# Optimization experiments

Hardware: AMD Instinct MI355X
Metric: run time of the kernel (lower is better)

The kernel has to match this reference:

```python
import jax, jax.numpy as jnp
import numpy as np

B, N1, N2, DEG = 64, 512, 512, 16
NF, NH, NL = 128, 128, 3
RATIO = 0.5
K1 = int(np.ceil(RATIO * N1))
K2 = int(np.ceil(RATIO * N2))
NCLS = 2
NCAT = NH * NL  # 384


def _gl(key, shape, fan_in):
    return jax.random.normal(key, shape, jnp.float32) / np.sqrt(fan_in)


def setup_inputs() -> dict:
    key = jax.random.key(0)
    ks = jax.random.split(key, 24)
    x = jax.random.normal(ks[0], (B * (N1 + N2), NF), jnp.float32)
    # edges within each component of each graph (c1-local / c2-local and global indexing)
    s1 = jax.random.randint(ks[1], (B, N1 * DEG), 0, N1)
    d1 = jax.random.randint(ks[2], (B, N1 * DEG), 0, N1)
    s2 = jax.random.randint(ks[3], (B, N2 * DEG), 0, N2)
    d2 = jax.random.randint(ks[4], (B, N2 * DEG), 0, N2)
    off1 = (jnp.arange(B) * N1)[:, None]
    off2 = (jnp.arange(B) * N2)[:, None]
    offg = (jnp.arange(B) * (N1 + N2))[:, None]
    src_c1 = (s1 + off1).reshape(-1).astype(jnp.int32)
    dst_c1 = (d1 + off1).reshape(-1).astype(jnp.int32)
    src_c2 = (s2 + off2).reshape(-1).astype(jnp.int32)
    dst_c2 = (d2 + off2).reshape(-1).astype(jnp.int32)
    src_all = jnp.concatenate([(s1 + offg).reshape(-1), (s2 + N1 + offg).reshape(-1)]).astype(jnp.int32)
    dst_all = jnp.concatenate([(d1 + offg).reshape(-1), (d2 + N1 + offg).reshape(-1)]).astype(jnp.int32)
    return {
        'x': x,
        'src_all': src_all, 'dst_all': dst_all,
        'src_c1': src_c1, 'dst_c1': dst_c1,
        'src_c2': src_c2, 'dst_c2': dst_c2,
        'W1': _gl(ks[5], (NF, NH), NF), 'b1': jnp.zeros((NH,), jnp.float32),
        'W2': _gl(ks[6], (NH, NH), NH), 'b2': jnp.zeros((NH,), jnp.float32),
        'W3': _gl(ks[7], (NH, NH), NH), 'b3': jnp.zeros((NH,), jnp.float32),
        'Wg_att': _gl(ks[8], (NCAT, NCAT), NCAT),
        'Wal': _gl(ks[9], (2 * NCAT, 2 * NCAT), 2 * NCAT), 'bal': jnp.zeros((2 * NCAT,), jnp.float32),
        'Wf': _gl(ks[10], (NCAT, NH), NCAT), 'bf': jnp.zeros((NH,), jnp.float32),
        'Wg_fin': _gl(ks[11], (NH, NH), NH),
        'Wl1': _gl(ks[12], (2 * NH, NH), 2 * NH), 'bl1': jnp.zeros((NH,), jnp.float32),
        'Wl2': _gl(ks[13], (NH, NH // 2), NH), 'bl2': jnp.zeros((NH // 2,), jnp.float32),
        'Wl3': _gl(ks[14], (NH // 2, NCLS), NH // 2), 'bl3': jnp.zeros((NCLS,), jnp.float32),
    }


def gcn_conv(x, src, dst, emask, W, b, n):
    # PyG GCNConv: symmetric norm with self-loops; masked edges contribute zero.
    xw = x @ W
    w = emask.astype(x.dtype)
    src_s = jnp.where(emask, src, 0)
    dst_s = jnp.where(emask, dst, 0)
    deg = jax.ops.segment_sum(w, dst_s, num_segments=n) + 1.0  # +1 self-loop
    dis = jax.lax.rsqrt(deg)
    norm = dis[src_s] * dis[dst_s] * w
    out = jax.ops.segment_sum(xw[src_s] * norm[:, None], dst_s, num_segments=n)
    out = out + xw * (dis * dis)[:, None]  # self-loop message
    return out + b


def att_pool(x, batch, counts, Wg, nseg):
    # global_pool with cfg 'ATT': gap -> tanh(W) -> broadcast -> sigmoid gate -> sum pool
    mean = jax.ops.segment_sum(x, batch, num_segments=nseg) / counts[:, None]
    c = jnp.tanh(mean @ Wg)
    alpha = jax.nn.sigmoid(jnp.sum(x * c[batch], axis=1, keepdims=True))
    return jax.ops.segment_sum(x * alpha, batch, num_segments=nseg)


def cag_pool(xc, src, dst, pv, n_per, k):
    # CAGPool_layer: score = <x, pool_vec>/||pool_vec||, per-graph topk, gate by sigmoid(score)
    batch = jnp.repeat(jnp.arange(B), n_per)
    x_ = pv[batch]
    score = jnp.sum(xc * x_, axis=1) / jnp.linalg.norm(x_, axis=1)
    order = jnp.argsort(-score.reshape(B, n_per), axis=1)[:, :k]
    perm = (order + (jnp.arange(B) * n_per)[:, None]).reshape(-1)  # [B*k]
    pooled = xc[perm] * jax.nn.sigmoid(score[perm])[:, None]
    # filter_adj: remap kept nodes, mask out edges touching dropped nodes
    node_map = jnp.full((B * n_per,), -1, dtype=jnp.int32).at[perm].set(jnp.arange(B * k, dtype=jnp.int32))
    r, c = node_map[src], node_map[dst]
    emask = (r >= 0) & (c >= 0)
    return pooled, r, c, emask


def reference(x, src_all, dst_all, src_c1, dst_c1, src_c2, dst_c2,
              W1, b1, W2, b2, W3, b3, Wg_att, Wal, bal, Wf, bf, Wg_fin,
              Wl1, bl1, Wl2, bl2, Wl3, bl3):
    N = B * (N1 + N2)
    ones_all = jnp.ones(src_all.shape[0], dtype=bool)
    h = jax.nn.relu(gcn_conv(x, src_all, dst_all, ones_all, W1, b1, N))
    xs = [h]
    for W, b in ((W2, b2), (W3, b3)):
        h = jax.nn.relu(gcn_conv(h, src_all, dst_all, ones_all, W, b, N))
        xs.append(h)
    xcat = jnp.concatenate(xs, axis=1)  # [N, NCAT]
    # split combined node set into c1 / c2 components (static layout)
    offg = (jnp.arange(B) * (N1 + N2))[:, None]
    idx1 = (offg + jnp.arange(N1)[None, :]).reshape(-1)
    idx2 = (offg + N1 + jnp.arange(N2)[None, :]).reshape(-1)
    x_c1, x_c2 = xcat[idx1], xcat[idx2]
    batch_c1 = jnp.repeat(jnp.arange(B), N1)
    batch_c2 = jnp.repeat(jnp.arange(B), N2)
    x12 = jnp.concatenate([x_c1, x_c2], axis=0)
    batch_ = jnp.concatenate([batch_c1, batch_c2 + B])
    counts = jnp.concatenate([jnp.full((B,), N1, jnp.float32), jnp.full((B,), N2, jnp.float32)])
    gp = att_pool(x12, batch_, counts, Wg_att, 2 * B)
    pv = jnp.concatenate([gp[:B], gp[B:]], axis=1) @ Wal + bal  # att_lin
    pv1, pv2 = pv[:, :NCAT], pv[:, NCAT:]
    p1, r1, c1e, m1 = cag_pool(x_c1, src_c1, dst_c1, pv1, N1, K1)
    p2, r2, c2e, m2 = cag_pool(x_c2, src_c2, dst_c2, pv2, N2, K2)
    h1 = jax.nn.relu(gcn_conv(p1, r1, c1e, m1, Wf, bf, B * K1))
    h2 = jax.nn.relu(gcn_conv(p2, r2, c2e, m2, Wf, bf, B * K2))
    g1 = att_pool(h1, jnp.repeat(jnp.arange(B), K1), jnp.full((B,), K1, jnp.float32), Wg_fin, B)
    g2 = att_pool(h2, jnp.repeat(jnp.arange(B), K2), jnp.full((B,), K2, jnp.float32), Wg_fin, B)
    pred = jnp.concatenate([g1, g2], axis=1)
    pred = jax.nn.relu(pred @ Wl1 + bl1)
    pred = jax.nn.relu(pred @ Wl2 + bl2)
    return pred @ Wl3 + bl3  # [B, NCLS]
```

## Files before the change

kernel.cpp:

```cpp
#include <hip/hip_runtime.h>
#include <math.h>

constexpr int BB   = 64;
constexpr int NPB  = 1024;
constexpr int NN   = BB * NPB;
constexpr int EALL = 1048576;
constexpr int EC   = 524288;
constexpr int EPG  = 8192;
constexpr int KTOP = 256;
constexpr int NP   = BB * KTOP;
constexpr int NP2  = 2 * NP;

__device__ __forceinline__ int wswz(int q) { return q ^ ((q >> 3) & 1); }

__global__ __launch_bounds__(256) void k_build_csr(const int* __restrict__ src_all,
                                                   const int* __restrict__ dst_all,
                                                   int* __restrict__ rowstart,
                                                   int* __restrict__ csrc,
                                                   float* __restrict__ dis) {
    __shared__ int cnt[512];
    __shared__ int rs[512];
    __shared__ int wsum[4];
    __shared__ int stage[EPG];
    const int g = blockIdx.x;
    const int b = g >> 1, c = g & 1;
    const int ebase  = c * EC + b * EPG;
    const int region = g * EPG;
    const int nbase  = g * 512;
    const int t = threadIdx.x;
    const int lane = t & 63, w = t >> 6;

    cnt[t] = 0; cnt[t + 256] = 0;
    __syncthreads();
    for (int i = 0; i < 32; i++) {
        int d = dst_all[ebase + t + 256 * i] & 511;
        atomicAdd(&cnt[d], 1);
    }
    __syncthreads();
    int v0 = cnt[2 * t], v1 = cnt[2 * t + 1];
    int p = v0 + v1;
    int incl = p;
    for (int off = 1; off < 64; off <<= 1) {
        int u = __shfl_up(incl, off);
        if (lane >= off) incl += u;
    }
    if (lane == 63) wsum[w] = incl;
    __syncthreads();
    int base = 0;
    for (int i = 0; i < w; i++) base += wsum[i];
    int excl = base + incl - p;
    rs[2 * t] = excl;
    rs[2 * t + 1] = excl + v0;
    rowstart[nbase + 2 * t]     = region + excl;
    rowstart[nbase + 2 * t + 1] = region + excl + v0;
    dis[nbase + 2 * t]     = 1.0f / sqrtf((float)v0 + 1.0f);
    dis[nbase + 2 * t + 1] = 1.0f / sqrtf((float)v1 + 1.0f);
    if (g == 127 && t == 0) rowstart[NN] = EALL;
    __syncthreads();
    for (int i = 0; i < 32; i++) {
        int e = ebase + t + 256 * i;
        int d = dst_all[e] & 511;
        int pp = atomicAdd(&rs[d], 1);
        stage[pp] = src_all[e];
    }
    __syncthreads();
    for (int i = 0; i < 32; i++)
        csrc[region + t + 256 * i] = stage[t + 256 * i];
}

__global__ __launch_bounds__(256) void k_build_csr_pooled(const int* __restrict__ s1,
                                                          const int* __restrict__ d1,
                                                          const int* __restrict__ s2,
                                                          const int* __restrict__ d2,
                                                          const int* __restrict__ nmap,
                                                          int* __restrict__ rowstart,
                                                          int* __restrict__ cntp,
                                                          int* __restrict__ csre,
                                                          float* __restrict__ disp) {
    __shared__ int cnt[256];
    __shared__ int rs[256];
    __shared__ int wsum[4];
    __shared__ int stage[EPG];
    const int g = blockIdx.x;
    const int c = g >> 6, b = g & 63;
    const int* ss = c ? s2 : s1;
    const int* dd = c ? d2 : d1;
    const int* nm = nmap + c * 32768;
    const int ebase  = b * EPG;
    const int region = g * EPG;
    const int nbase  = g * 256;
    const int t = threadIdx.x;
    const int lane = t & 63, w = t >> 6;

    cnt[t] = 0;
    __syncthreads();
    for (int i = 0; i < 32; i++) {
        int e = ebase + t + 256 * i;
        int r = nm[ss[e]], cc = nm[dd[e]];
        if (r >= 0 && cc >= 0) atomicAdd(&cnt[cc & 255], 1);
    }
    __syncthreads();
    int v = cnt[t];
    int incl = v;
    for (int off = 1; off < 64; off <<= 1) {
        int u = __shfl_up(incl, off);
        if (lane >= off) incl += u;
    }
    if (lane == 63) wsum[w] = incl;
    __syncthreads();
    int base = 0;
    for (int i = 0; i < w; i++) base += wsum[i];
    int excl = base + incl - v;
    rs[t] = excl;
    rowstart[nbase + t] = region + excl;
    cntp[nbase + t] = v;
    disp[nbase + t] = 1.0f / sqrtf((float)v + 1.0f);
    __syncthreads();
    for (int i = 0; i < 32; i++) {
        int e = ebase + t + 256 * i;
        int r = nm[ss[e]], cc = nm[dd[e]];
        if (r >= 0 && cc >= 0) {
            int pp = atomicAdd(&rs[cc & 255], 1);
            stage[pp] = r;
        }
    }
    __syncthreads();
    for (int i = 0; i < 32; i++)
        csre[region + t + 256 * i] = stage[t + 256 * i];
}

template <int KDIM>
__global__ __launch_bounds__(256) void k_gemm_tile(const float* __restrict__ A, int lda,
                                                   const float* __restrict__ W,
                                                   const float* __restrict__ rowscale,
                                                   float* __restrict__ C, int M) {
    __shared__ float As[32][136];
    __shared__ float Ws[32 * 128];
    const int tid  = threadIdx.x;
    const int c0 = (tid & 15) * 8;
    const int r0 = (tid >> 4) * 8;
    const int row0 = blockIdx.x * 128;
    const int arow = tid >> 1;
    const int aq   = tid & 1;

    float acc[8][8];
#pragma unroll
    for (int i = 0; i < 8; i++)
#pragma unroll
        for (int j = 0; j < 8; j++) acc[i][j] = 0.f;

    for (int k0 = 0; k0 < KDIM; k0 += 32) {
        __syncthreads();
        const float* Ap = A + (size_t)(row0 + arow) * lda + k0;
#pragma unroll
        for (int qq = 0; qq < 4; qq++) {
            int kk = (aq + 2 * qq) * 4;
            float4 av = *(const float4*)(Ap + kk);
            As[kk + 0][arow] = av.x;
            As[kk + 1][arow] = av.y;
            As[kk + 2][arow] = av.z;
            As[kk + 3][arow] = av.w;
        }
#pragma unroll
        for (int q = 0; q < 4; q++) {
            int f = tid + 256 * q;
            int kk = f >> 5, qd = f & 31;
            float4 wv = *(const float4*)(W + (size_t)k0 * 128 + f * 4);
            *(float4*)&Ws[kk * 128 + wswz(qd) * 4] = wv;
        }
        __syncthreads();
#pragma unroll 2
        for (int kk = 0; kk < 32; kk++) {
            int q0 = c0 >> 2;
            float4 a0 = *(const float4*)&As[kk][r0];
            float4 a1 = *(const float4*)&As[kk][r0 + 4];
            float4 b0 = *(const float4*)&Ws[kk * 128 + wswz(q0) * 4];
            float4 b1 = *(const float4*)&Ws[kk * 128 + wswz(q0 + 1) * 4];
            float a[8] = {a0.x, a0.y, a0.z, a0.w, a1.x, a1.y, a1.z, a1.w};
            float b[8] = {b0.x, b0.y, b0.z, b0.w, b1.x, b1.y, b1.z, b1.w};
#pragma unroll
            for (int i = 0; i < 8; i++)
#pragma unroll
                for (int j = 0; j < 8; j++)
                    acc[i][j] = fmaf(a[i], b[j], acc[i][j]);
        }
    }
#pragma unroll
    for (int i = 0; i < 8; i++) {
        int row = row0 + r0 + i;
        if (row < M) {
            float sc = rowscale[row];
            float4 o0 = {acc[i][0]*sc, acc[i][1]*sc, acc[i][2]*sc, acc[i][3]*sc};
            float4 o1 = {acc[i][4]*sc, acc[i][5]*sc, acc[i][6]*sc, acc[i][7]*sc};
            *(float4*)(C + (size_t)row * 128 + c0) = o0;
            *(float4*)(C + (size_t)row * 128 + c0 + 4) = o1;
        }
    }
}

__global__ __launch_bounds__(512) void k_gemm_gather(const float* __restrict__ XC,
                                                     const int* __restrict__ sel,
                                                     const float* __restrict__ SC,
                                                     const float* __restrict__ rowscale,
                                                     const float* __restrict__ W,
                                                     float* __restrict__ C) {
    __shared__ float As[32][136];
    __shared__ float Ws[32 * 128];
    const int tid  = threadIdx.x;
    const int c0 = (tid & 15) * 8;
    const int r0 = (tid >> 4) * 4;
    const int row0 = blockIdx.x * 128;
    const int arow = tid >> 2;
    const int aq   = tid & 3;

    int n = row0 + arow;
    int comm = n >= NP;
    int nl = n - (comm ? NP : 0);
    int b = nl >> 8;
    int old = sel[n];
    const float* srow = XC + (size_t)(b * NPB + comm * 512 + old) * 384;
    float scv = SC[comm * 32768 + b * 512 + old];
    float sg = 1.f / (1.f + expf(-scv));

    float acc[4][8];
#pragma unroll
    for (int i = 0; i < 4; i++)
#pragma unroll
        for (int j = 0; j < 8; j++) acc[i][j] = 0.f;

    for (int k0 = 0; k0 < 384; k0 += 32) {
        __syncthreads();
#pragma unroll
        for (int qq = 0; qq < 2; qq++) {
            int kk = (aq + 4 * qq) * 4;
            float4 av = *(const float4*)(srow + k0 + kk);
            As[kk + 0][arow] = av.x * sg;
            As[kk + 1][arow] = av.y * sg;
            As[kk + 2][arow] = av.z * sg;
            As[kk + 3][arow] = av.w * sg;
        }
#pragma unroll
        for (int q = 0; q < 2; q++) {
            int f = tid + 512 * q;
            int kk = f >> 5, qd = f & 31;
            float4 wv = *(const float4*)(W + (size_t)k0 * 128 + f * 4);
            *(float4*)&Ws[kk * 128 + wswz(qd) * 4] = wv;
        }
        __syncthreads();
#pragma unroll 2
        for (int kk = 0; kk < 32; kk++) {
            int q0 = c0 >> 2;
            float4 a0 = *(const float4*)&As[kk][r0];
            float4 b0 = *(const float4*)&Ws[kk * 128 + wswz(q0) * 4];
            float4 b1 = *(const float4*)&Ws[kk * 128 + wswz(q0 + 1) * 4];
            float a[4] = {a0.x, a0.y, a0.z, a0.w};
            float b8[8] = {b0.x, b0.y, b0.z, b0.w, b1.x, b1.y, b1.z, b1.w};
#pragma unroll
            for (int i = 0; i < 4; i++)
#pragma unroll
                for (int j = 0; j < 8; j++)
                    acc[i][j] = fmaf(a[i], b8[j], acc[i][j]);
        }
    }
#pragma unroll
    for (int i = 0; i < 4; i++) {
        int row = row0 + r0 + i;
        float sc = rowscale[row];
        float4 o0 = {acc[i][0]*sc, acc[i][1]*sc, acc[i][2]*sc, acc[i][3]*sc};
        float4 o1 = {acc[i][4]*sc, acc[i][5]*sc, acc[i][6]*sc, acc[i][7]*sc};
        *(float4*)(C + (size_t)row * 128 + c0) = o0;
        *(float4*)(C + (size_t)row * 128 + c0 + 4) = o1;
    }
}

__global__ void k_aggregate4(const float* __restrict__ xwsc, const float* __restrict__ dis,
                             const int* __restrict__ rowstart, const int* __restrict__ csrc,
                             const float* __restrict__ bias, float* __restrict__ XC, int colbase) {
    int xcd  = blockIdx.x & 7;
    int slot = blockIdx.x >> 3;
    int g    = ((slot >> 6) << 3) | xcd;
    int node = g * 512 + (slot & 63) * 8 + (threadIdx.x >> 5);
    int l    = threadIdx.x & 31;
    const float4* xw4 = (const float4*)xwsc;
    float4 acc = xw4[(size_t)node * 32 + l];
    int e0 = rowstart[node], e1 = rowstart[node + 1];
    for (int e = e0; e < e1; e++) {
        int s = csrc[e];
        float4 u = xw4[(size_t)s * 32 + l];
        acc.x += u.x; acc.y += u.y; acc.z += u.z; acc.w += u.w;
    }
    float di = dis[node];
    float4 b4 = ((const float4*)bias)[l];
    acc.x = fmaxf(acc.x * di + b4.x, 0.f);
    acc.y = fmaxf(acc.y * di + b4.y, 0.f);
    acc.z = fmaxf(acc.z * di + b4.z, 0.f);
    acc.w = fmaxf(acc.w * di + b4.w, 0.f);
    *(float4*)(XC + (size_t)node * 384 + colbase + l * 4) = acc;
}

__global__ void k_aggregate_pooled(const float* __restrict__ xwsc, const float* __restrict__ disp,
                                   const int* __restrict__ rowstart, const int* __restrict__ cntp,
                                   const int* __restrict__ csre,
                                   const float* __restrict__ bias, float* __restrict__ H) {
    int xcd  = blockIdx.x & 7;
    int slot = blockIdx.x >> 3;
    int g    = ((slot >> 5) << 3) | xcd;
    int node = g * 256 + (slot & 31) * 8 + (threadIdx.x >> 5);
    int l    = threadIdx.x & 31;
    const float4* xw4 = (const float4*)xwsc;
    float4 acc = xw4[(size_t)node * 32 + l];
    int e0 = rowstart[node], n = cntp[node];
    for (int i = 0; i < n; i++) {
        int r = csre[e0 + i];
        float4 u = xw4[(size_t)r * 32 + l];
        acc.x += u.x; acc.y += u.y; acc.z += u.z; acc.w += u.w;
    }
    float di = disp[node];
    float4 b4 = ((const float4*)bias)[l];
    acc.x = fmaxf(acc.x * di + b4.x, 0.f);
    acc.y = fmaxf(acc.y * di + b4.y, 0.f);
    acc.z = fmaxf(acc.z * di + b4.z, 0.f);
    acc.w = fmaxf(acc.w * di + b4.w, 0.f);
    *(float4*)(H + (size_t)node * 128 + l * 4) = acc;
}

__global__ void k_mean_part(const float* __restrict__ XC, float* __restrict__ mpart) {
    int blk = blockIdx.x;
    int gc = blk >> 2, p = blk & 3;
    int seg = ((gc & 1) << 6) | (gc >> 1);
    int c = threadIdx.x;
    int base = gc * 512 + p * 128;
    float s = 0.f;
    for (int i = 0; i < 128; i++) s += XC[(size_t)(base + i) * 384 + c];
    mpart[(size_t)(seg * 4 + p) * 384 + c] = s;
}

__global__ void k_c12(const float* __restrict__ mpart, const float* __restrict__ Wg,
                      float* __restrict__ c12) {
    __shared__ float ms[384];
    int seg = blockIdx.x; int c = threadIdx.x;
    ms[c] = (mpart[(size_t)(seg * 4 + 0) * 384 + c] + mpart[(size_t)(seg * 4 + 1) * 384 + c] +
             mpart[(size_t)(seg * 4 + 2) * 384 + c] + mpart[(size_t)(seg * 4 + 3) * 384 + c]) *
            (1.0f / 512.0f);
    __syncthreads();
    float s = 0.f;
    for (int k = 0; k < 384; k++) s = fmaf(ms[k], Wg[(size_t)k * 384 + c], s);
    c12[seg * 384 + c] = tanhf(s);
}

__global__ __launch_bounds__(256) void k_attpool1(const float* __restrict__ XC,
                                                  const float* __restrict__ C12,
                                                  float* __restrict__ GP) {
    __shared__ float gps[4][384];
    int blk = blockIdx.x;
    int gc = blk >> 2, q = blk & 3;
    int seg = ((gc & 1) << 6) | (gc >> 1);
    int w = threadIdx.x >> 6, l = threadIdx.x & 63;
    const float* c12r = C12 + seg * 384;
    float4 cr0 = *(const float4*)(c12r + 4 * l);
    float4 cr1 = (l < 32) ? *(const float4*)(c12r + 256 + 4 * l) : float4{0.f,0.f,0.f,0.f};
    float4 a0 = {0.f,0.f,0.f,0.f}, a1 = {0.f,0.f,0.f,0.f};
    int base = gc * 512 + q * 128 + w * 32;
    for (int it = 0; it < 32; it++) {
        const float* xr = XC + (size_t)(base + it) * 384;
        float4 v0 = *(const float4*)(xr + 4 * l);
        float4 v1 = (l < 32) ? *(const float4*)(xr + 256 + 4 * l) : float4{0.f,0.f,0.f,0.f};
        float s = v0.x*cr0.x + v0.y*cr0.y + v0.z*cr0.z + v0.w*cr0.w
                + v1.x*cr1.x + v1.y*cr1.y + v1.z*cr1.z + v1.w*cr1.w;
        for (int off = 32; off; off >>= 1) s += __shfl_xor(s, off);
        float al = 1.f / (1.f + expf(-s));
        a0.x += v0.x*al; a0.y += v0.y*al; a0.z += v0.z*al; a0.w += v0.w*al;
        a1.x += v1.x*al; a1.y += v1.y*al; a1.z += v1.z*al; a1.w += v1.w*al;
    }
    *(float4*)&gps[w][4 * l] = a0;
    if (l < 32) *(float4*)&gps[w][256 + 4 * l] = a1;
    __syncthreads();
    for (int c = threadIdx.x; c < 384; c += 256) {
        float s = gps[0][c] + gps[1][c] + gps[2][c] + gps[3][c];
        atomicAdd(&GP[seg * 384 + c], s);
    }
}

__global__ void k_pv(const float* __restrict__ gp, const float* __restrict__ Wal,
                     const float* __restrict__ bal, float* __restrict__ pv) {
    int row = blockIdx.x;
    int c   = threadIdx.x;
    float s = bal[c];
    for (int k = 0; k < 768; k++) {
        float v = (k < 384) ? gp[row * 384 + k] : gp[(64 + row) * 384 + (k - 384)];
        s = fmaf(v, Wal[(size_t)k * 768 + c], s);
    }
    pv[row * 768 + c] = s;
}

__global__ void k_pnorm(const float* __restrict__ pv, float* __restrict__ pnorm) {
    int id = blockIdx.x;
    int lane = threadIdx.x;
    int h = id >> 6, b = id & 63;
    const float* p = pv + b * 768 + h * 384;
    float s = 0.f;
    for (int k = lane; k < 384; k += 64) s += p[k] * p[k];
    for (int off = 32; off; off >>= 1) s += __shfl_down(s, off);
    if (lane == 0) pnorm[id] = sqrtf(s);
}

__global__ void k_score(const float* __restrict__ XC, const float* __restrict__ pv,
                        const float* __restrict__ pnorm, float* __restrict__ sc) {
    int nl2 = blockIdx.x * 4 + (threadIdx.x >> 6);
    int lane = threadIdx.x & 63;
    int comm = nl2 >> 15;
    int nl = nl2 & 32767;
    int b = nl >> 9; int i = nl & 511;
    const float* xr = XC + (size_t)(b * NPB + comm * 512 + i) * 384;
    const float* pr = pv + b * 768 + comm * 384;
    float4 x0 = *(const float4*)(xr + 4 * lane);
    float4 p0 = *(const float4*)(pr + 4 * lane);
    float s = x0.x*p0.x + x0.y*p0.y + x0.z*p0.z + x0.w*p0.w;
    if (lane < 32) {
        float4 x1 = *(const float4*)(xr + 256 + 4 * lane);
        float4 p1 = *(const float4*)(pr + 256 + 4 * lane);
        s += x1.x*p1.x + x1.y*p1.y + x1.z*p1.z + x1.w*p1.w;
    }
    for (int off = 32; off; off >>= 1) s += __shfl_down(s, off);
    if (lane == 0) sc[comm * 32768 + nl] = s / pnorm[comm * 64 + b];
}

__global__ void k_topk(const float* __restrict__ sc, int* __restrict__ sel, int* __restrict__ nmap) {
    __shared__ float sv[512];
    __shared__ int   si[512];
    int blk = blockIdx.x;
    int t = threadIdx.x;
    sv[t] = sc[blk * 512 + t];             si[t] = t;
    sv[t + 256] = sc[blk * 512 + t + 256]; si[t + 256] = t + 256;
    __syncthreads();
    for (int k2 = 2; k2 <= 512; k2 <<= 1) {
        for (int j = k2 >> 1; j > 0; j >>= 1) {
            for (int i = t; i < 512; i += 256) {
                int l = i ^ j;
                if (l > i) {
                    bool desc = ((i & k2) == 0);
                    float a = sv[i], bb2 = sv[l];
                    bool sw = desc ? (a < bb2) : (a > bb2);
                    if (sw) {
                        sv[i] = bb2; sv[l] = a;
                        int tmp = si[i]; si[i] = si[l]; si[l] = tmp;
                    }
                }
            }
            __syncthreads();
        }
    }
    sel[blk * 256 + t] = si[t];
    nmap[blk * 512 + si[t]] = blk * 256 + t;
    nmap[blk * 512 + si[t + 256]] = -1;
}

__global__ void k_meanf(const float* __restrict__ H, float* __restrict__ mean) {
    int b = blockIdx.x; int c = threadIdx.x;
    float s = 0.f;
    for (int i = 0; i < 256; i++) s += H[(size_t)(b * 256 + i) * 128 + c];
    mean[b * 128 + c] = s * (1.0f / 256.0f);
}

__global__ void k_cfin(const float* __restrict__ mean, const float* __restrict__ Wg,
                       float* __restrict__ cf) {
    __shared__ float ms[128];
    int b = blockIdx.x; int c = threadIdx.x;
    ms[c] = mean[b * 128 + c];
    __syncthreads();
    float s = 0.f;
    for (int k = 0; k < 128; k++) s = fmaf(ms[k], Wg[k * 128 + c], s);
    cf[b * 128 + c] = tanhf(s);
}

__global__ void k_alphaf(const float* __restrict__ H, const float* __restrict__ cf,
                         float* __restrict__ al) {
    int node = blockIdx.x * 4 + (threadIdx.x >> 6);
    int lane = threadIdx.x & 63;
    int b = node >> 8;
    float s = 0.f;
    if (lane < 32) {
        float4 h = *(const float4*)(H + (size_t)node * 128 + 4 * lane);
        float4 c = *(const float4*)(cf + b * 128 + 4 * lane);
        s = h.x*c.x + h.y*c.y + h.z*c.z + h.w*c.w;
    }
    for (int off = 32; off; off >>= 1) s += __shfl_down(s, off);
    if (lane == 0) al[node] = 1.f / (1.f + expf(-s));
}

__global__ void k_gfin(const float* __restrict__ H, const float* __restrict__ al,
                       float* __restrict__ g) {
    int seg = blockIdx.x; int c = threadIdx.x;
    int b = seg & 63, comm = seg >> 6;
    float s = 0.f;
    for (int i = 0; i < 256; i++) { int n = seg * 256 + i; s += H[(size_t)n * 128 + c] * al[n]; }
    g[b * 256 + comm * 128 + c] = s;
}

__global__ void k_mlp(const float* __restrict__ G,
                      const float* __restrict__ Wl1, const float* __restrict__ bl1,
                      const float* __restrict__ Wl2, const float* __restrict__ bl2,
                      const float* __restrict__ Wl3, const float* __restrict__ bl3,
                      float* __restrict__ out) {
    __shared__ float t1[128], t2[64];
    int b = blockIdx.x; int t = threadIdx.x;
    float s = bl1[t];
    for (int k = 0; k < 256; k++) s = fmaf(G[b * 256 + k], Wl1[k * 128 + t], s);
    t1[t] = fmaxf(s, 0.f);
    __syncthreads();
    if (t < 64) {
        float s2 = bl2[t];
        for (int k = 0; k < 128; k++) s2 = fmaf(t1[k], Wl2[k * 64 + t], s2);
        t2[t] = fmaxf(s2, 0.f);
    }
    __syncthreads();
    if (t < 2) {
        float s3 = bl3[t];
        for (int k = 0; k < 64; k++) s3 = fmaf(t2[k], Wl3[k * 2 + t], s3);
        out[b * 2 + t] = s3;
    }
}

extern "C" void kernel_launch(void* const* d_in, const int* in_sizes, int n_in,
                              void* d_out, int out_size, void* d_ws, size_t ws_size,
                              hipStream_t stream) {
    const float* x       = (const float*)d_in[0];
    const int*   src_all = (const int*)d_in[1];
    const int*   dst_all = (const int*)d_in[2];
    const int*   src_c1  = (const int*)d_in[3];
    const int*   dst_c1  = (const int*)d_in[4];
    const int*   src_c2  = (const int*)d_in[5];
    const int*   dst_c2  = (const int*)d_in[6];
    const float* W1 = (const float*)d_in[7];   const float* b1 = (const float*)d_in[8];
    const float* W2 = (const float*)d_in[9];   const float* b2 = (const float*)d_in[10];
    const float* W3 = (const float*)d_in[11];  const float* b3 = (const float*)d_in[12];
    const float* Wg_att = (const float*)d_in[13];
    const float* Wal = (const float*)d_in[14]; const float* bal = (const float*)d_in[15];
    const float* Wf  = (const float*)d_in[16]; const float* bf  = (const float*)d_in[17];
    const float* Wg_fin = (const float*)d_in[18];
    const float* Wl1 = (const float*)d_in[19]; const float* bl1 = (const float*)d_in[20];
    const float* Wl2 = (const float*)d_in[21]; const float* bl2 = (const float*)d_in[22];
    const float* Wl3 = (const float*)d_in[23]; const float* bl3 = (const float*)d_in[24];
    float* out = (float*)d_out;

    float* f = (float*)d_ws;
    size_t o = 0;
    float* XC   = f + o; o += (size_t)NN * 384;
    float* SCR  = f + o; o += (size_t)NN * 128;
    float* H    = f + o; o += (size_t)NP2 * 128;
    int* ROWSTART = (int*)(f + o); o += 65552;
    int* CSRC     = (int*)(f + o); o += EALL;
    int* CNTP     = (int*)(f + o); o += NP2;
    float* DIS    = f + o; o += NN;
    float* MPART  = f + o; o += 512 * 384;
    float* C12    = f + o; o += 128 * 384;
    float* GP     = f + o; o += 128 * 384;
    float* PV     = f + o; o += 64 * 768;
    float* PNORM  = f + o; o += 128;
    float* SC     = f + o; o += 65536;
    int* SEL      = (int*)(f + o); o += NP2;
    int* NMAP     = (int*)(f + o); o += 65536;
    float* DISP   = f + o; o += NP2;
    float* MEANF  = f + o; o += 128 * 128;
    float* CFIN   = f + o; o += 128 * 128;
    float* ALF    = f + o; o += NP2;
    float* G12    = f + o; o += 64 * 256;
    size_t needed_bytes = o * sizeof(float);
    if (ws_size < needed_bytes) return;

    float* XWP = SCR;

    k_build_csr<<<128, 256, 0, stream>>>(src_all, dst_all, ROWSTART, CSRC, DIS);

    k_gemm_tile<128><<<NN / 128, 256, 0, stream>>>(x, 128, W1, DIS, SCR, NN);
    k_aggregate4<<<NN / 8, 256, 0, stream>>>(SCR, DIS, ROWSTART, CSRC, b1, XC, 0);
    k_gemm_tile<128><<<NN / 128, 256, 0, stream>>>(XC + 0, 384, W2, DIS, SCR, NN);
    k_aggregate4<<<NN / 8, 256, 0, stream>>>(SCR, DIS, ROWSTART, CSRC, b2, XC, 128);
    k_gemm_tile<128><<<NN / 128, 256, 0, stream>>>(XC + 128, 384, W3, DIS, SCR, NN);
    k_aggregate4<<<NN / 8, 256, 0, stream>>>(SCR, DIS, ROWSTART, CSRC, b3, XC, 256);

    k_mean_part<<<512, 384, 0, stream>>>(XC, MPART);
    k_c12<<<128, 384, 0, stream>>>(MPART, Wg_att, C12);
    hipMemsetAsync(GP, 0, 128 * 384 * sizeof(float), stream);
    k_attpool1<<<512, 256, 0, stream>>>(XC, C12, GP);
    k_pv<<<64, 768, 0, stream>>>(GP, Wal, bal, PV);
    k_pnorm<<<128, 64, 0, stream>>>(PV, PNORM);

    k_score<<<65536 / 4, 256, 0, stream>>>(XC, PV, PNORM, SC);
    k_topk<<<128, 256, 0, stream>>>(SC, SEL, NMAP);

    k_build_csr_pooled<<<128, 256, 0, stream>>>(src_c1, dst_c1, src_c2, dst_c2,
                                                NMAP, ROWSTART, CNTP, CSRC, DISP);

    k_gemm_gather<<<NP2 / 128, 512, 0, stream>>>(XC, SEL, SC, DISP, Wf, XWP);
    k_aggregate_pooled<<<NP2 / 8, 256, 0, stream>>>(XWP, DISP, ROWSTART, CNTP, CSRC, bf, H);

    k_meanf<<<128, 128, 0, stream>>>(H, MEANF);
    k_cfin<<<128, 128, 0, stream>>>(MEANF, Wg_fin, CFIN);
    k_alphaf<<<NP2 / 4, 256, 0, stream>>>(H, CFIN, ALF);
    k_gfin<<<128, 128, 0, stream>>>(H, ALF, G12);

    k_mlp<<<64, 128, 0, stream>>>(G12, Wl1, bl1, Wl2, bl2, Wl3, bl3, out);
}
```

Measured before the change: 631.1 us.

## Double-buffer shared-memory tiles with register prefetch in GEMM kernels

Both tiled GEMM kernels now use two shared-memory buffers. The next K-tile is loaded from global memory into registers while the current tile is computed, then written to the other buffer, so there is one barrier per iteration instead of two. The W swizzle becomes a full XOR (q ^ (q>>3)) and the A padding drops from 136 to 132 to change the LDS bank mapping. This doubles LDS use and adds prefetch registers, which may lower occupancy.

```diff
diff --git a/kernel.cpp b/kernel.cpp
--- a/kernel.cpp
+++ b/kernel.cpp
@@ -11,7 +11,7 @@
 constexpr int NP   = BB * KTOP;
 constexpr int NP2  = 2 * NP;
 
-__device__ __forceinline__ int wswz(int q) { return q ^ ((q >> 3) & 1); }
+__device__ __forceinline__ int pq(int q) { return q ^ (q >> 3); }
 
 __global__ __launch_bounds__(256) void k_build_csr(const int* __restrict__ src_all,
                                                    const int* __restrict__ dst_all,
@@ -134,14 +134,17 @@
                                                    const float* __restrict__ W,
                                                    const float* __restrict__ rowscale,
                                                    float* __restrict__ C, int M) {
-    __shared__ float As[32][136];
-    __shared__ float Ws[32 * 128];
+    __shared__ float As[2][32][132];
+    __shared__ float Ws[2][32 * 128];
     const int tid  = threadIdx.x;
     const int c0 = (tid & 15) * 8;
     const int r0 = (tid >> 4) * 8;
     const int row0 = blockIdx.x * 128;
     const int arow = tid >> 1;
     const int aq   = tid & 1;
+    const float* Ap = A + (size_t)(row0 + arow) * lda;
+    const int pq0 = pq(c0 >> 2) * 4;
+    const int pq1 = pq((c0 >> 2) + 1) * 4;
 
     float acc[8][8];
 #pragma unroll
@@ -149,33 +152,50 @@
 #pragma unroll
         for (int j = 0; j < 8; j++) acc[i][j] = 0.f;
 
-    for (int k0 = 0; k0 < KDIM; k0 += 32) {
-        __syncthreads();
-        const float* Ap = A + (size_t)(row0 + arow) * lda + k0;
-#pragma unroll
-        for (int qq = 0; qq < 4; qq++) {
-            int kk = (aq + 2 * qq) * 4;
-            float4 av = *(const float4*)(Ap + kk);
-            As[kk + 0][arow] = av.x;
-            As[kk + 1][arow] = av.y;
-            As[kk + 2][arow] = av.z;
-            As[kk + 3][arow] = av.w;
-        }
-#pragma unroll
-        for (int q = 0; q < 4; q++) {
-            int f = tid + 256 * q;
-            int kk = f >> 5, qd = f & 31;
-            float4 wv = *(const float4*)(W + (size_t)k0 * 128 + f * 4);
-            *(float4*)&Ws[kk * 128 + wswz(qd) * 4] = wv;
-        }
-        __syncthreads();
+    float4 areg[4], wreg[4];
+#pragma unroll
+    for (int qq = 0; qq < 4; qq++)
+        areg[qq] = *(const float4*)(Ap + (aq + 2 * qq) * 4);
+#pragma unroll
+    for (int q = 0; q < 4; q++) {
+        int f = tid + 256 * q;
+        wreg[q] = *(const float4*)(W + (size_t)(f >> 5) * 128 + (f & 31) * 4);
+    }
+#pragma unroll
+    for (int qq = 0; qq < 4; qq++) {
+        int kk = (aq + 2 * qq) * 4;
+        As[0][kk + 0][arow] = areg[qq].x;
+        As[0][kk + 1][arow] = areg[qq].y;
+        As[0][kk + 2][arow] = areg[qq].z;
+        As[0][kk + 3][arow] = areg[qq].w;
+    }
+#pragma unroll
+    for (int q = 0; q < 4; q++) {
+        int f = tid + 256 * q;
+        *(float4*)&Ws[0][(f >> 5) * 128 + pq(f & 31) * 4] = wreg[q];
+    }
+    __syncthreads();
+
+    constexpr int NT = KDIM / 32;
+    for (int t = 0; t < NT; t++) {
+        const int cur = t & 1;
+        if (t + 1 < NT) {
+            int k0 = (t + 1) * 32;
+#pragma unroll
+            for (int qq = 0; qq < 4; qq++)
+                areg[qq] = *(const float4*)(Ap + k0 + (aq + 2 * qq) * 4);
+#pragma unroll
+            for (int q = 0; q < 4; q++) {
+                int f = tid + 256 * q;
+                wreg[q] = *(const float4*)(W + (size_t)(k0 + (f >> 5)) * 128 + (f & 31) * 4);
+            }
+        }
 #pragma unroll 2
         for (int kk = 0; kk < 32; kk++) {
-            int q0 = c0 >> 2;
-            float4 a0 = *(const float4*)&As[kk][r0];
-            float4 a1 = *(const float4*)&As[kk][r0 + 4];
-            float4 b0 = *(const float4*)&Ws[kk * 128 + wswz(q0) * 4];
-            float4 b1 = *(const float4*)&Ws[kk * 128 + wswz(q0 + 1) * 4];
+            float4 a0 = *(const float4*)&As[cur][kk][r0];
+            float4 a1 = *(const float4*)&As[cur][kk][r0 + 4];
+            float4 b0 = *(const float4*)&Ws[cur][kk * 128 + pq0];
+            float4 b1 = *(const float4*)&Ws[cur][kk * 128 + pq1];
             float a[8] = {a0.x, a0.y, a0.z, a0.w, a1.x, a1.y, a1.z, a1.w};
             float b[8] = {b0.x, b0.y, b0.z, b0.w, b1.x, b1.y, b1.z, b1.w};
 #pragma unroll
@@ -184,6 +204,23 @@
                 for (int j = 0; j < 8; j++)
                     acc[i][j] = fmaf(a[i], b[j], acc[i][j]);
         }
+        if (t + 1 < NT) {
+            const int nxt = cur ^ 1;
+#pragma unroll
+            for (int qq = 0; qq < 4; qq++) {
+                int kk = (aq + 2 * qq) * 4;
+                As[nxt][kk + 0][arow] = areg[qq].x;
+                As[nxt][kk + 1][arow] = areg[qq].y;
+                As[nxt][kk + 2][arow] = areg[qq].z;
+                As[nxt][kk + 3][arow] = areg[qq].w;
+            }
+#pragma unroll
+            for (int q = 0; q < 4; q++) {
+                int f = tid + 256 * q;
+                *(float4*)&Ws[nxt][(f >> 5) * 128 + pq(f & 31) * 4] = wreg[q];
+            }
+        }
+        __syncthreads();
     }
 #pragma unroll
     for (int i = 0; i < 8; i++) {
@@ -204,14 +241,16 @@
                                                      const float* __restrict__ rowscale,
                                                      const float* __restrict__ W,
                                                      float* __restrict__ C) {
-    __shared__ float As[32][136];
-    __shared__ float Ws[32 * 128];
+    __shared__ float As[2][32][132];
+    __shared__ float Ws[2][32 * 128];
     const int tid  = threadIdx.x;
     const int c0 = (tid & 15) * 8;
     const int r0 = (tid >> 4) * 4;
     const int row0 = blockIdx.x * 128;
     const int arow = tid >> 2;
     const int aq   = tid & 3;
+    const int pq0 = pq(c0 >> 2) * 4;
+    const int pq1 = pq((c0 >> 2) + 1) * 4;
 
     int n = row0 + arow;
     int comm = n >= NP;
@@ -228,31 +267,49 @@
 #pragma unroll
         for (int j = 0; j < 8; j++) acc[i][j] = 0.f;
 
-    for (int k0 = 0; k0 < 384; k0 += 32) {
-        __syncthreads();
-#pragma unroll
-        for (int qq = 0; qq < 2; qq++) {
-            int kk = (aq + 4 * qq) * 4;
-            float4 av = *(const float4*)(srow + k0 + kk);
-            As[kk + 0][arow] = av.x * sg;
-            As[kk + 1][arow] = av.y * sg;
-            As[kk + 2][arow] = av.z * sg;
-            As[kk + 3][arow] = av.w * sg;
-        }
-#pragma unroll
-        for (int q = 0; q < 2; q++) {
-            int f = tid + 512 * q;
-            int kk = f >> 5, qd = f & 31;
-            float4 wv = *(const float4*)(W + (size_t)k0 * 128 + f * 4);
-            *(float4*)&Ws[kk * 128 + wswz(qd) * 4] = wv;
-        }
-        __syncthreads();
+    float4 areg[2], wreg[2];
+#pragma unroll
+    for (int qq = 0; qq < 2; qq++)
+        areg[qq] = *(const float4*)(srow + (aq + 4 * qq) * 4);
+#pragma unroll
+    for (int q = 0; q < 2; q++) {
+        int f = tid + 512 * q;
+        wreg[q] = *(const float4*)(W + (size_t)(f >> 5) * 128 + (f & 31) * 4);
+    }
+#pragma unroll
+    for (int qq = 0; qq < 2; qq++) {
+        int kk = (aq + 4 * qq) * 4;
+        As[0][kk + 0][arow] = areg[qq].x * sg;
+        As[0][kk + 1][arow] = areg[qq].y * sg;
+        As[0][kk + 2][arow] = areg[qq].z * sg;
+        As[0][kk + 3][arow] = areg[qq].w * sg;
+    }
+#pragma unroll
+    for (int q = 0; q < 2; q++) {
+        int f = tid + 512 * q;
+        *(float4*)&Ws[0][(f >> 5) * 128 + pq(f & 31) * 4] = wreg[q];
+    }
+    __syncthreads();
+
+    constexpr int NT = 12;
+    for (int t = 0; t < NT; t++) {
+        const int cur = t & 1;
+        if (t + 1 < NT) {
+            int k0 = (t + 1) * 32;
+#pragma unroll
+            for (int qq = 0; qq < 2; qq++)
+                areg[qq] = *(const float4*)(srow + k0 + (aq + 4 * qq) * 4);
+#pragma unroll
+            for (int q = 0; q < 2; q++) {
+                int f = tid + 512 * q;
+                wreg[q] = *(const float4*)(W + (size_t)(k0 + (f >> 5)) * 128 + (f & 31) * 4);
+            }
+        }
 #pragma unroll 2
         for (int kk = 0; kk < 32; kk++) {
-            int q0 = c0 >> 2;
-            float4 a0 = *(const float4*)&As[kk][r0];
-            float4 b0 = *(const float4*)&Ws[kk * 128 + wswz(q0) * 4];
-            float4 b1 = *(const float4*)&Ws[kk * 128 + wswz(q0 + 1) * 4];
+            float4 a0 = *(const float4*)&As[cur][kk][r0];
+            float4 b0 = *(const float4*)&Ws[cur][kk * 128 + pq0];
+            float4 b1 = *(const float4*)&Ws[cur][kk * 128 + pq1];
             float a[4] = {a0.x, a0.y, a0.z, a0.w};
             float b8[8] = {b0.x, b0.y, b0.z, b0.w, b1.x, b1.y, b1.z, b1.w};
 #pragma unroll
@@ -261,6 +318,23 @@
                 for (int j = 0; j < 8; j++)
                     acc[i][j] = fmaf(a[i], b8[j], acc[i][j]);
         }
+        if (t + 1 < NT) {
+            const int nxt = cur ^ 1;
+#pragma unroll
+            for (int qq = 0; qq < 2; qq++) {
+                int kk = (aq + 4 * qq) * 4;
+                As[nxt][kk + 0][arow] = areg[qq].x * sg;
+                As[nxt][kk + 1][arow] = areg[qq].y * sg;
+                As[nxt][kk + 2][arow] = areg[qq].z * sg;
+                As[nxt][kk + 3][arow] = areg[qq].w * sg;
+            }
+#pragma unroll
+            for (int q = 0; q < 2; q++) {
+                int f = tid + 512 * q;
+                *(float4*)&Ws[nxt][(f >> 5) * 128 + pq(f & 31) * 4] = wreg[q];
+            }
+        }
+        __syncthreads();
     }
 #pragma unroll
     for (int i = 0; i < 4; i++) {
```

New measurement: 659.0 us. 4.4% more time.
